# Performance work log

Measured on AMD Instinct MI355X. Metric: run time of the kernel, lower is better.

## Reference

```python
import jax, jax.numpy as jnp
import numpy as np

# ---- static problem constants ----
LX, LY, D, P = 6, 6, 4, 2          # PEPS grid, bond dim, phys dim
CHI = 16                            # max_bond for boundary truncation
ETA = 0.1                           # nn_eta
NS = LX * LY                        # n_sites = 36
E, HEADS, HID = 128, 8, 512         # embed_dim, attn_heads, nn_hidden_dim
B = 2048                            # batch

def _shapes():
    s = []
    for i in range(LX):
        for j in range(LY):
            s.append((1 if i == 0 else D, 1 if i == LX - 1 else D,
                      1 if j == 0 else D, 1 if j == LY - 1 else D, P))
    return s

SHAPES = _shapes()                              # per-site (u,d,l,r,p)
SIZES = [int(np.prod(s)) for s in SHAPES]       # param_sizes in PointwiseBackflow
OFFS = np.concatenate([[0], np.cumsum(SIZES)])
TOTAL = int(OFFS[-1])
MAXS = max(SIZES)                               # 512


def setup_inputs() -> dict:
    key = jax.random.key(0)
    ks = jax.random.split(key, 12)
    f = jnp.float32
    return {
        "x": jax.random.randint(ks[0], (B, NS), 0, P),
        "ftn_flat": jax.random.normal(ks[1], (TOTAL,), f) * 0.25,
        "emb": jax.random.normal(ks[2], (P, E), f) * 0.1,
        "pos": jax.random.normal(ks[3], (NS, E), f) * 0.1,
        "Wqkv": jax.random.normal(ks[4], (E, 3 * E), f) / np.sqrt(E),
        "bqkv": jnp.zeros((3 * E,), f),
        "Wo": jax.random.normal(ks[5], (E, E), f) / np.sqrt(E),
        "bo": jnp.zeros((E,), f),
        "W1": jax.random.normal(ks[6], (E, HID), f) / np.sqrt(E),
        "b1": jnp.zeros((HID,), f),
        "W2": jax.random.normal(ks[7], (HID, MAXS), f) * 0.02,
        "b2": jnp.zeros((MAXS,), f),
    }


def _compress(mps, chi):
    """Canonicalize (top->bottom) then SVD-truncate (bottom->top) an open MPS.
    mps[i] has shape (bond_up, bond_down, phys); cutoff=0, max_bond=chi."""
    mps = list(mps)
    n = len(mps)
    for i in range(n - 1):
        a, b, p = mps[i].shape
        U, S, Vh = jnp.linalg.svd(mps[i].transpose(0, 2, 1).reshape(a * p, b),
                                  full_matrices=False)
        k = U.shape[1]
        mps[i] = U.reshape(a, p, k).transpose(0, 2, 1)
        mps[i + 1] = jnp.einsum('kb,bcp->kcp', S[:, None] * Vh, mps[i + 1])
    for i in range(n - 1, 0, -1):
        a, b, p = mps[i].shape
        U, S, Vh = jnp.linalg.svd(mps[i].reshape(a, b * p), full_matrices=False)
        k = min(chi, int(S.shape[0]))
        mps[i] = Vh[:k].reshape(k, b, p)
        mps[i - 1] = jnp.einsum('xap,ak->xkp', mps[i - 1], U[:, :k] * S[:k])
    return mps


def _absorb(bt, t, side):
    # bt: (a, c, q) boundary-MPS tensor, t: (u, d, l, r) site tensor
    if side == 'r':   # contract q with site's l, new phys = r
        out = jnp.einsum('acl,udlr->aucdr', bt, t)
    else:             # contract q with site's r, new phys = l
        out = jnp.einsum('acr,udlr->aucdl', bt, t)
    a, u, c, d, p = out.shape
    return out.reshape(a * u, c * d, p)


def _contract_one(xi, vec):
    """Amplitude of one config: select phys indices, then boundary contraction
    from ymin over cols [0, LY//2-1] and from ymax over cols [LY//2, LY-1]."""
    grid = []
    for i in range(LX):
        row = []
        for j in range(LY):
            k_ = i * LY + j
            t = vec[OFFS[k_]:OFFS[k_ + 1]].reshape(SHAPES[k_])
            row.append(jnp.take(t, xi[k_], axis=-1))  # (u,d,l,r)
        grid.append(row)
    # left boundary MPS (phys = right bond)
    lmps = [grid[i][0][:, :, 0, :] for i in range(LX)]
    for j in range(1, LY // 2):
        lmps = _compress([_absorb(lmps[i], grid[i][j], 'r') for i in range(LX)], CHI)
    # right boundary MPS (phys = left bond)
    rmps = [grid[i][LY - 1][:, :, :, 0] for i in range(LX)]
    for j in range(LY - 2, LY // 2 - 1, -1):
        rmps = _compress([_absorb(rmps[i], grid[i][j], 'l') for i in range(LX)], CHI)
    # zip the two boundary MPS
    M = jnp.ones((1, 1), vec.dtype)
    for i in range(LX):
        M = jnp.einsum('xy,xap,ybp->ab', M, lmps[i], rmps[i])
    return M[0, 0]


def _forward(x, ftn_flat, emb, pos, Wqkv, bqkv, Wo, bo, W1, b1, W2, b2):
    bsz = x.shape[0]
    h = emb[x] + pos                                   # [B, NS, E]
    qkv = h @ Wqkv + bqkv
    q, k, v = jnp.split(qkv, 3, axis=-1)
    dh = E // HEADS
    q = q.reshape(bsz, NS, HEADS, dh)
    k = k.reshape(bsz, NS, HEADS, dh)
    v = v.reshape(bsz, NS, HEADS, dh)
    att = jax.nn.softmax(jnp.einsum('bqhd,bkhd->bhqk', q, k) / np.sqrt(dh), axis=-1)
    o = jnp.einsum('bhqk,bkhd->bqhd', att, v).reshape(bsz, NS, E)
    h = h + o @ Wo + bo                                # attn block output
    raw = jax.nn.gelu(h @ W1 + b1, approximate=False) @ W2 + b2  # [B, NS, MAXS]
    # PointwiseBackflow: per-site trim + concat
    nn_out = jnp.concatenate([raw[:, i, :SIZES[i]] for i in range(NS)], axis=1)
    vecs = ftn_flat[None, :] + ETA * nn_out            # [B, TOTAL]
    return jax.vmap(_contract_one)(x, vecs)            # [B]


def reference(x, ftn_flat, emb, pos, Wqkv, bqkv, Wo, bo, W1, b1, W2, b2):
    return _forward(x, ftn_flat, emb, pos, Wqkv, bqkv, Wo, bo, W1, b1, W2, b2)
```

## Files before the change

### kernel.cpp

```cpp
#include <hip/hip_runtime.h>
#include <math.h>


#define BSZ   2048
#define NS    36
#define EMB   128
#define NHEAD 8
#define DH    16
#define HIDD  512
#define TOTV  10368

typedef float f16v __attribute__((ext_vector_type(16)));

__device__ __forceinline__ float hsum16(f16v v) {
    float a = (v[0] + v[1]) + (v[2] + v[3]);
    float b = (v[4] + v[5]) + (v[6] + v[7]);
    float c = (v[8] + v[9]) + (v[10] + v[11]);
    float d = (v[12] + v[13]) + (v[14] + v[15]);
    return (a + b) + (c + d);
}

__constant__ int c_offs[37] = {
    0,32,160,288,416,544,576,
    704,1216,1728,2240,2752,2880,
    3008,3520,4032,4544,5056,5184,
    5312,5824,6336,6848,7360,7488,
    7616,8128,8640,9152,9664,9792,
    9824,9952,10080,10208,10336,10368};

__constant__ int c_ps[84] = {
    0,1,2,3,4,5,
    6,7,7,7,7,8,8,8,8,9,9,9,9,10,10,10,10,11,
    12,13,13,13,13,14,14,14,14,15,15,15,15,16,16,16,16,17,
    18,19,19,19,19,20,20,20,20,21,21,21,21,22,22,22,22,23,
    24,25,25,25,25,26,26,26,26,27,27,27,27,28,28,28,28,29,
    30,31,32,33,34,35};
__constant__ int c_pc[84] = {
    0,0,0,0,0,0,
    0,0,1,2,3,0,1,2,3,0,1,2,3,0,1,2,3,0,
    0,0,1,2,3,0,1,2,3,0,1,2,3,0,1,2,3,0,
    0,0,1,2,3,0,1,2,3,0,1,2,3,0,1,2,3,0,
    0,0,1,2,3,0,1,2,3,0,1,2,3,0,1,2,3,0,
    0,0,0,0,0,0};

__global__ __launch_bounds__(256) void k_embed(const int* __restrict__ x,
        const float* __restrict__ emb, const float* __restrict__ pos,
        float* __restrict__ h) {
    int idx = blockIdx.x * 256 + threadIdx.x;
    if (idx >= BSZ * NS * EMB) return;
    int e = idx & (EMB - 1);
    int g = idx >> 7;
    int s = g % NS;
    h[idx] = emb[x[g] * EMB + e] + pos[s * EMB + e];
}

__global__ __launch_bounds__(256) void k_qkv(const float* __restrict__ h,
        const float* __restrict__ Wqkv, const float* __restrict__ bqkv,
        float* __restrict__ qkv) {
    __shared__ float As[64 * 132];
    __shared__ float Ws[32 * 132];
    int tid = threadIdx.x;
    int chunk = blockIdx.x;
    int tok0 = blockIdx.y * 64;
    int tx = tid & 15, ty = tid >> 4;
    for (int idx = tid; idx < 64 * 128; idx += 256) {
        int t = idx >> 7, k = idx & 127;
        As[t * 132 + k] = h[(size_t)(tok0 + t) * EMB + k];
    }
    float acc[4][8];
    #pragma unroll
    for (int i = 0; i < 4; ++i)
        #pragma unroll
        for (int q = 0; q < 8; ++q) acc[i][q] = 0.f;
    for (int ks = 0; ks < 4; ++ks) {
        __syncthreads();
        for (int idx = tid; idx < 32 * 128; idx += 256) {
            int kk = idx >> 7, c = idx & 127;
            Ws[kk * 132 + c] = Wqkv[(size_t)(ks * 32 + kk) * 384 + chunk * 128 + c];
        }
        __syncthreads();
        #pragma unroll 4
        for (int kk = 0; kk < 32; ++kk) {
            float4 w0 = *(const float4*)&Ws[kk * 132 + tx * 8];
            float4 w1 = *(const float4*)&Ws[kk * 132 + tx * 8 + 4];
            #pragma unroll
            for (int i = 0; i < 4; ++i) {
                float a = As[(ty * 4 + i) * 132 + ks * 32 + kk];
                acc[i][0] += a * w0.x; acc[i][1] += a * w0.y;
                acc[i][2] += a * w0.z; acc[i][3] += a * w0.w;
                acc[i][4] += a * w1.x; acc[i][5] += a * w1.y;
                acc[i][6] += a * w1.z; acc[i][7] += a * w1.w;
            }
        }
    }
    #pragma unroll
    for (int i = 0; i < 4; ++i) {
        size_t base = (size_t)(tok0 + ty * 4 + i) * 384 + chunk * 128 + tx * 8;
        #pragma unroll
        for (int q = 0; q < 8; ++q)
            qkv[base + q] = acc[i][q] + bqkv[chunk * 128 + tx * 8 + q];
    }
}

__global__ __launch_bounds__(256) void k_attnc(float* __restrict__ qkv) {
    __shared__ float qs[4][NS * 17];
    __shared__ float ks_[4][NS * 17];
    __shared__ float vs[4][NS * 17];
    __shared__ float S[4][NS * 37];
    int wid = threadIdx.x >> 6, lane = threadIdx.x & 63;
    int m = blockIdx.x * 4 + wid;
    int b = m >> 3, hd = m & 7;
    float* Q = qkv + (size_t)b * NS * 384 + hd * DH;
    for (int idx = lane; idx < NS * DH; idx += 64) {
        int t = idx >> 4, d = idx & 15;
        qs[wid][t * 17 + d]  = Q[t * 384 + d];
        ks_[wid][t * 17 + d] = Q[t * 384 + 128 + d];
        vs[wid][t * 17 + d]  = Q[t * 384 + 256 + d];
    }
    __syncthreads();
    for (int idx = lane; idx < NS * NS; idx += 64) {
        int qp = idx / NS, kp = idx - qp * NS;
        float acc = 0.f;
        #pragma unroll
        for (int d = 0; d < DH; ++d)
            acc += qs[wid][qp * 17 + d] * ks_[wid][kp * 17 + d];
        S[wid][qp * 37 + kp] = acc * 0.25f;
    }
    __syncthreads();
    if (lane < NS) {
        float mx = -1e30f;
        for (int j = 0; j < NS; ++j) mx = fmaxf(mx, S[wid][lane * 37 + j]);
        float z = 0.f;
        for (int j = 0; j < NS; ++j) {
            float e = expf(S[wid][lane * 37 + j] - mx);
            S[wid][lane * 37 + j] = e; z += e;
        }
        float inv = 1.f / z;
        for (int j = 0; j < NS; ++j) S[wid][lane * 37 + j] *= inv;
    }
    __syncthreads();
    for (int idx = lane; idx < NS * DH; idx += 64) {
        int qp = idx >> 4, d = idx & 15;
        float acc = 0.f;
        for (int kp = 0; kp < NS; ++kp)
            acc += S[wid][qp * 37 + kp] * vs[wid][kp * 17 + d];
        Q[qp * 384 + d] = acc;
    }
}

__global__ __launch_bounds__(256) void k_oproj(const float* __restrict__ qkv,
        const float* __restrict__ Wo, const float* __restrict__ bo,
        float* __restrict__ h) {
    __shared__ float As[64 * 132];
    __shared__ float Ws[32 * 132];
    int tid = threadIdx.x;
    int tok0 = blockIdx.x * 64;
    int tx = tid & 15, ty = tid >> 4;
    for (int idx = tid; idx < 64 * 128; idx += 256) {
        int t = idx >> 7, k = idx & 127;
        As[t * 132 + k] = qkv[(size_t)(tok0 + t) * 384 + k];
    }
    float acc[4][8];
    #pragma unroll
    for (int i = 0; i < 4; ++i)
        #pragma unroll
        for (int q = 0; q < 8; ++q) acc[i][q] = 0.f;
    for (int ks = 0; ks < 4; ++ks) {
        __syncthreads();
        for (int idx = tid; idx < 32 * 128; idx += 256) {
            int kk = idx >> 7, c = idx & 127;
            Ws[kk * 132 + c] = Wo[(size_t)(ks * 32 + kk) * EMB + c];
        }
        __syncthreads();
        #pragma unroll 4
        for (int kk = 0; kk < 32; ++kk) {
            float4 w0 = *(const float4*)&Ws[kk * 132 + tx * 8];
            float4 w1 = *(const float4*)&Ws[kk * 132 + tx * 8 + 4];
            #pragma unroll
            for (int i = 0; i < 4; ++i) {
                float a = As[(ty * 4 + i) * 132 + ks * 32 + kk];
                acc[i][0] += a * w0.x; acc[i][1] += a * w0.y;
                acc[i][2] += a * w0.z; acc[i][3] += a * w0.w;
                acc[i][4] += a * w1.x; acc[i][5] += a * w1.y;
                acc[i][6] += a * w1.z; acc[i][7] += a * w1.w;
            }
        }
    }
    #pragma unroll
    for (int i = 0; i < 4; ++i) {
        size_t base = (size_t)(tok0 + ty * 4 + i) * EMB + tx * 8;
        #pragma unroll
        for (int q = 0; q < 8; ++q)
            h[base + q] = h[base + q] + acc[i][q] + bo[tx * 8 + q];
    }
}

__global__ __launch_bounds__(256) void k_gemm1(const float* __restrict__ h,
        const float* __restrict__ W1, const float* __restrict__ b1,
        float* __restrict__ Hm) {
    __shared__ float As[64 * 132];
    __shared__ float Ws[32 * 132];
    int tid = threadIdx.x;
    int chunk = blockIdx.x;
    int tok0 = blockIdx.y * 64;
    int tx = tid & 15, ty = tid >> 4;
    for (int idx = tid; idx < 64 * 128; idx += 256) {
        int t = idx >> 7, k = idx & 127;
        As[t * 132 + k] = h[(size_t)(tok0 + t) * EMB + k];
    }
    float acc[4][8];
    #pragma unroll
    for (int i = 0; i < 4; ++i)
        #pragma unroll
        for (int q = 0; q < 8; ++q) acc[i][q] = 0.f;
    for (int ks = 0; ks < 4; ++ks) {
        __syncthreads();
        for (int idx = tid; idx < 32 * 128; idx += 256) {
            int kk = idx >> 7, c = idx & 127;
            Ws[kk * 132 + c] = W1[(size_t)(ks * 32 + kk) * HIDD + chunk * 128 + c];
        }
        __syncthreads();
        #pragma unroll 4
        for (int kk = 0; kk < 32; ++kk) {
            float4 w0 = *(const float4*)&Ws[kk * 132 + tx * 8];
            float4 w1 = *(const float4*)&Ws[kk * 132 + tx * 8 + 4];
            #pragma unroll
            for (int i = 0; i < 4; ++i) {
                float a = As[(ty * 4 + i) * 132 + ks * 32 + kk];
                acc[i][0] += a * w0.x; acc[i][1] += a * w0.y;
                acc[i][2] += a * w0.z; acc[i][3] += a * w0.w;
                acc[i][4] += a * w1.x; acc[i][5] += a * w1.y;
                acc[i][6] += a * w1.z; acc[i][7] += a * w1.w;
            }
        }
    }
    #pragma unroll
    for (int i = 0; i < 4; ++i) {
        size_t base = (size_t)(tok0 + ty * 4 + i) * HIDD + chunk * 128 + tx * 8;
        #pragma unroll
        for (int q = 0; q < 8; ++q) {
            float a = acc[i][q] + b1[chunk * 128 + tx * 8 + q];
            Hm[base + q] = 0.5f * a * (1.f + erff(a * 0.70710678118654752f));
        }
    }
}

__global__ __launch_bounds__(256) void k_gemm2(const float* __restrict__ Hm,
        const float* __restrict__ W2, const float* __restrict__ b2,
        const float* __restrict__ ftn, float* __restrict__ vecs, int e8) {
    __shared__ float As[64 * 33];
    __shared__ float Ws[32 * 132];
    int tid = threadIdx.x;
    int pair = blockIdx.x;
    int s = c_ps[pair], chunk = c_pc[pair];
    int b0 = blockIdx.y * 64;
    int off = c_offs[s], size = c_offs[s + 1] - off;
    int tx = tid & 15, ty = tid >> 4;
    float acc[4][8];
    #pragma unroll
    for (int i = 0; i < 4; ++i)
        #pragma unroll
        for (int q = 0; q < 8; ++q) acc[i][q] = 0.f;
    for (int ks = 0; ks < 16; ++ks) {
        __syncthreads();
        for (int idx = tid; idx < 64 * 32; idx += 256) {
            int t = idx >> 5, kk = idx & 31;
            As[t * 33 + kk] = Hm[(size_t)((b0 + t) * NS + s) * HIDD + ks * 32 + kk];
        }
        for (int idx = tid; idx < 32 * 128; idx += 256) {
            int kk = idx >> 7, c = idx & 127;
            Ws[kk * 132 + c] = W2[(size_t)(ks * 32 + kk) * HIDD + chunk * 128 + c];
        }
        __syncthreads();
        #pragma unroll 4
        for (int kk = 0; kk < 32; ++kk) {
            float4 w0 = *(const float4*)&Ws[kk * 132 + tx * 8];
            float4 w1 = *(const float4*)&Ws[kk * 132 + tx * 8 + 4];
            #pragma unroll
            for (int i = 0; i < 4; ++i) {
                float a = As[(ty * 4 + i) * 33 + kk];
                acc[i][0] += a * w0.x; acc[i][1] += a * w0.y;
                acc[i][2] += a * w0.z; acc[i][3] += a * w0.w;
                acc[i][4] += a * w1.x; acc[i][5] += a * w1.y;
                acc[i][6] += a * w1.z; acc[i][7] += a * w1.w;
            }
        }
    }
    #pragma unroll
    for (int i = 0; i < 4; ++i) {
        int bg = e8 * 256 + b0 + ty * 4 + i;
        #pragma unroll
        for (int q = 0; q < 8; ++q) {
            int col = chunk * 128 + tx * 8 + q;
            if (col < size) {
                float o = acc[i][q] + b2[col];
                vecs[(size_t)bg * TOTV + off + col] = ftn[off + col] + 0.1f * o;
            }
        }
    }
}

__device__ __forceinline__ float* build_half(const float* __restrict__ vb,
        const int* __restrict__ xb, int side, int upper,
        float* cur, float* fre, float* ts0, float* ts1, float* ts2, int tid) {
    if (tid == 0) cur[0] = 1.0f;
    __syncthreads();
    int bd = 1, lgbd = 0;
    for (int t = 0; t < 3; ++t) {
        int xd = t ? 4 : 1, lgxd = t ? 2 : 0;
        int j = side ? (5 - t) : t;
        int rows[3];
        rows[0] = upper ? 0 : 5; rows[1] = upper ? 1 : 4; rows[2] = upper ? 2 : 3;
        for (int role = 0; role < 3; ++role) {
            int i = rows[role];
            int dd = (i < 5) ? 4 : 1, dl = (j > 0) ? 4 : 1, dr = (j < 5) ? 4 : 1;
            int su = dd * dl * dr * 2, sd = dl * dr * 2, sl = dr * 2, sr = 2;
            int xstr = side ? sr : sl, ystr = side ? sl : sr;
            int base = c_offs[i * 6 + j] + xb[i * 6 + j];
            if (role == 0) {
                int astr = upper ? sd : su;
                int n = 4 * xd * 4;
                for (int idx = tid; idx < n; idx += 256) {
                    int y = idx & 3, xx = (idx >> 2) & (xd - 1), a = idx >> (2 + lgxd);
                    ts0[idx] = vb[base + a * astr + xx * xstr + y * ystr];
                }
            } else if (role == 1) {
                int astr = upper ? su : sd, cstr = upper ? sd : su;
                int n = 16 * xd * 4;
                for (int idx = tid; idx < n; idx += 256) {
                    int y = idx & 3, xx = (idx >> 2) & (xd - 1);
                    int c = (idx >> (2 + lgxd)) & 3, a = idx >> (4 + lgxd);
                    ts1[idx] = vb[base + a * astr + c * cstr + xx * xstr + y * ystr];
                }
            } else {
                int cstr = upper ? su : sd, bstr = upper ? sd : su;
                int n = 16 * xd * 4;
                for (int idx = tid; idx < n; idx += 256) {
                    int y = idx & 3, xx = (idx >> 2) & (xd - 1);
                    int bb = (idx >> (2 + lgxd)) & 3, c = idx >> (4 + lgxd);
                    ts2[idx] = vb[base + c * cstr + bb * bstr + xx * xstr + y * ystr];
                }
            }
        }
        __syncthreads();
        int n1 = 16 * xd * xd * bd;
        for (int idx = tid; idx < n1; idx += 256) {
            int bt = idx & (bd - 1);
            int r = idx >> lgbd;
            int x2 = r & (xd - 1); r >>= lgxd;
            int x1 = r & (xd - 1); r >>= lgxd;
            int a = r & 3, y0 = r >> 2;
            float s2 = 0.f;
            for (int x0 = 0; x0 < xd; ++x0)
                s2 += cur[(((((x0 << lgxd) | x1) << lgxd) | x2) << lgbd) | bt]
                    * ts0[(((a << lgxd) | x0) << 2) | y0];
            fre[idx] = s2;
        }
        __syncthreads();
        int n2 = 64 * xd * bd;
        for (int idx = tid; idx < n2; idx += 256) {
            int bt = idx & (bd - 1);
            int r = idx >> lgbd;
            int x2 = r & (xd - 1); r >>= lgxd;
            int c = r & 3, y1 = (r >> 2) & 3, y0 = r >> 4;
            float s2 = 0.f;
            for (int a = 0; a < 4; ++a)
                for (int x1 = 0; x1 < xd; ++x1)
                    s2 += fre[((((((((y0 << 2) | a) << lgxd) | x1) << lgxd) | x2)) << lgbd) | bt]
                        * ts1[((((a * 4 + c) << lgxd) | x1) << 2) | y1];
            cur[idx] = s2;
        }
        __syncthreads();
        int n3 = 256 * bd;
        for (int idx = tid; idx < n3; idx += 256) {
            int bn = idx & (4 * bd - 1);
            int bt = bn >> 2, bb = bn & 3;
            int r = idx >> (lgbd + 2);
            int y2 = r & 3, y1 = (r >> 2) & 3, y0 = r >> 4;
            float s2 = 0.f;
            for (int c = 0; c < 4; ++c)
                for (int x2 = 0; x2 < xd; ++x2)
                    s2 += cur[((((((y0 << 2) | y1) << 2 | c) << lgxd) | x2) << lgbd) | bt]
                        * ts2[((((c * 4 + bb) << lgxd) | x2) << 2) | y2];
            fre[idx] = s2;
        }
        __syncthreads();
        float* tmp = cur; cur = fre; fre = tmp;
        bd <<= 2; lgbd += 2;
    }
    return cur;
}

__global__ __launch_bounds__(256) void k_build(const float* __restrict__ vecs,
        const int* __restrict__ x, float* __restrict__ psi) {
    __shared__ float X1[4096], X2[4096], X3[4096];
    __shared__ float ts0[64], ts1[256], ts2[256];
    int m = blockIdx.x;
    int b = m >> 1, side = m & 1;
    int tid = threadIdx.x;
    const float* vb = vecs + (size_t)b * TOTV;
    const int* xb = x + b * NS;
    float* A  = build_half(vb, xb, side, 1, X1, X2, ts0, ts1, ts2, tid);
    float* Bt = build_half(vb, xb, side, 0, X1, X3, ts0, ts1, ts2, tid);
    float* po = psi + (size_t)m * 4096;
    for (int idx = tid; idx < 4096; idx += 256) {
        int u = idx >> 6, l = idx & 63;
        const float4* a4 = (const float4*)(A + u * 64);
        const float4* b4 = (const float4*)(Bt + l * 64);
        float s2 = 0.f;
        #pragma unroll
        for (int q = 0; q < 16; ++q) {
            float4 av = a4[q], bv = b4[q];
            s2 += av.x * bv.x + av.y * bv.y + av.z * bv.z + av.w * bv.w;
        }
        po[idx] = s2;
    }
}

__global__ __launch_bounds__(64, 1) void k_svd(const float* __restrict__ psi,
                                               float* __restrict__ wv) {
    __shared__ __align__(16) float qlds[2][64 * 20];
    int lane = threadIdx.x;
    int mA = blockIdx.x * 2;
    const float* PA = psi + (size_t)mA * 4096;
    const float* PB = PA + 4096;
    f16v a0, a1, a2, a3, b0, b1, b2, b3;
    #pragma unroll
    for (int r = 0; r < 16; ++r) a0[r] = PA[r * 64 + lane];
    #pragma unroll
    for (int r = 0; r < 16; ++r) a1[r] = PA[(r + 16) * 64 + lane];
    #pragma unroll
    for (int r = 0; r < 16; ++r) a2[r] = PA[(r + 32) * 64 + lane];
    #pragma unroll
    for (int r = 0; r < 16; ++r) a3[r] = PA[(r + 48) * 64 + lane];
    #pragma unroll
    for (int r = 0; r < 16; ++r) b0[r] = PB[r * 64 + lane];
    #pragma unroll
    for (int r = 0; r < 16; ++r) b1[r] = PB[(r + 16) * 64 + lane];
    #pragma unroll
    for (int r = 0; r < 16; ++r) b2[r] = PB[(r + 32) * 64 + lane];
    #pragma unroll
    for (int r = 0; r < 16; ++r) b3[r] = PB[(r + 48) * 64 + lane];

    bool actA = true, actB = true;
    for (int sweep = 0; sweep < 5; ++sweep) {
        if (!actA && !actB) break;
        float nA = 0.f, nB = 0.f;
        if (actA) {
            f16v nv = a0 * a0 + a1 * a1 + a2 * a2 + a3 * a3;
            nA = hsum16(nv);
        }
        if (actB) {
            f16v nv = b0 * b0 + b1 * b1 + b2 * b2 + b3 * b3;
            nB = hsum16(nv);
        }
        bool bigA = false, bigB = false;
        for (int mm = 1; mm < 64; ++mm) {
            int partner = lane ^ mm;
            if (actA) {
                f16v p0, p1, p2, p3;
                #pragma unroll
                for (int r = 0; r < 16; ++r) p0[r] = __shfl(a0[r], partner);
                #pragma unroll
                for (int r = 0; r < 16; ++r) p1[r] = __shfl(a1[r], partner);
                #pragma unroll
                for (int r = 0; r < 16; ++r) p2[r] = __shfl(a2[r], partner);
                #pragma unroll
                for (int r = 0; r < 16; ++r) p3[r] = __shfl(a3[r], partner);
                f16v gv = a0 * p0 + a1 * p1 + a2 * p2 + a3 * p3;
                float gam = hsum16(gv);
                float beta2 = __shfl(nA, partner);
                float scale = sqrtf(fmaxf(nA * beta2, 0.f));
                bool rot = fabsf(gam) > 1e-5f * scale;
                bool big = fabsf(gam) > 4e-3f * scale;
                if (__ballot(big) != 0ull) bigA = true;
                if (__ballot(rot) != 0ull) {
                    float c = 1.f, s = 0.f;
                    if (rot) {
                        float zeta = (nA - beta2) / (2.f * gam);
                        float sgn = (zeta > 0.f) ? 1.f :
                                    ((zeta < 0.f) ? -1.f : ((lane < partner) ? 1.f : -1.f));
                        float tt = sgn / (fabsf(zeta) + sqrtf(1.f + zeta * zeta));
                        c = 1.f / sqrtf(1.f + tt * tt);
                        s = c * tt;
                    }
                    a0 = c * a0 + s * p0;
                    a1 = c * a1 + s * p1;
                    a2 = c * a2 + s * p2;
                    a3 = c * a3 + s * p3;
                    nA = c * c * nA + s * s * beta2 + 2.f * c * s * gam;
                }
            }
            if (actB) {
                f16v p0, p1, p2, p3;
                #pragma unroll
                for (int r = 0; r < 16; ++r) p0[r] = __shfl(b0[r], partner);
                #pragma unroll
                for (int r = 0; r < 16; ++r) p1[r] = __shfl(b1[r], partner);
                #pragma unroll
                for (int r = 0; r < 16; ++r) p2[r] = __shfl(b2[r], partner);
                #pragma unroll
                for (int r = 0; r < 16; ++r) p3[r] = __shfl(b3[r], partner);
                f16v gv = b0 * p0 + b1 * p1 + b2 * p2 + b3 * p3;
                float gam = hsum16(gv);
                float beta2 = __shfl(nB, partner);
                float scale = sqrtf(fmaxf(nB * beta2, 0.f));
                bool rot = fabsf(gam) > 1e-5f * scale;
                bool big = fabsf(gam) > 4e-3f * scale;
                if (__ballot(big) != 0ull) bigB = true;
                if (__ballot(rot) != 0ull) {
                    float c = 1.f, s = 0.f;
                    if (rot) {
                        float zeta = (nB - beta2) / (2.f * gam);
                        float sgn = (zeta > 0.f) ? 1.f :
                                    ((zeta < 0.f) ? -1.f : ((lane < partner) ? 1.f : -1.f));
                        float tt = sgn / (fabsf(zeta) + sqrtf(1.f + zeta * zeta));
                        c = 1.f / sqrtf(1.f + tt * tt);
                        s = c * tt;
                    }
                    b0 = c * b0 + s * p0;
                    b1 = c * b1 + s * p1;
                    b2 = c * b2 + s * p2;
                    b3 = c * b3 + s * p3;
                    nB = c * c * nB + s * s * beta2 + 2.f * c * s * gam;
                }
            }
        }
        actA = actA && bigA;
        actB = actB && bigB;
    }

    {
        f16v ne = a0 * a0 + a1 * a1 + a2 * a2 + a3 * a3;
        float n2e = hsum16(ne);
        int rank = 0;
        for (int j = 0; j < 64; ++j) {
            float nj = __shfl(n2e, j);
            if (nj > n2e || (nj == n2e && j < lane)) ++rank;
        }
        float inv = (n2e > 1e-30f) ? 1.f / sqrtf(n2e) : 0.f;
        if (rank < 16) {
            #pragma unroll
            for (int r = 0; r < 16; ++r) {
                qlds[0][r * 20 + rank]        = a0[r] * inv;
                qlds[0][(r + 16) * 20 + rank] = a1[r] * inv;
                qlds[0][(r + 32) * 20 + rank] = a2[r] * inv;
                qlds[0][(r + 48) * 20 + rank] = a3[r] * inv;
            }
        }
    }
    {
        f16v ne = b0 * b0 + b1 * b1 + b2 * b2 + b3 * b3;
        float n2e = hsum16(ne);
        int rank = 0;
        for (int j = 0; j < 64; ++j) {
            float nj = __shfl(n2e, j);
            if (nj > n2e || (nj == n2e && j < lane)) ++rank;
        }
        float inv = (n2e > 1e-30f) ? 1.f / sqrtf(n2e) : 0.f;
        if (rank < 16) {
            #pragma unroll
            for (int r = 0; r < 16; ++r) {
                qlds[1][r * 20 + rank]        = b0[r] * inv;
                qlds[1][(r + 16) * 20 + rank] = b1[r] * inv;
                qlds[1][(r + 32) * 20 + rank] = b2[r] * inv;
                qlds[1][(r + 48) * 20 + rank] = b3[r] * inv;
            }
        }
    }
    __syncthreads();
    #pragma unroll
    for (int g = 0; g < 2; ++g) {
        const float* P = g ? PB : PA;
        float* o = wv + (size_t)(mA + g) * 2048;
        #pragma unroll
        for (int k = 0; k < 16; ++k) o[k * 64 + lane] = qlds[g][lane * 20 + k];
        f16v t;
        #pragma unroll
        for (int k = 0; k < 16; ++k) t[k] = 0.f;
        for (int r = 0; r < 64; ++r) {
            float pr = P[r * 64 + lane];
            const float4* q4 = (const float4*)&qlds[g][r * 20];
            float4 a = q4[0], b = q4[1], cc = q4[2], d = q4[3];
            t[0]  += a.x  * pr; t[1]  += a.y  * pr; t[2]  += a.z  * pr; t[3]  += a.w  * pr;
            t[4]  += b.x  * pr; t[5]  += b.y  * pr; t[6]  += b.z  * pr; t[7]  += b.w  * pr;
            t[8]  += cc.x * pr; t[9]  += cc.y * pr; t[10] += cc.z * pr; t[11] += cc.w * pr;
            t[12] += d.x  * pr; t[13] += d.y  * pr; t[14] += d.z  * pr; t[15] += d.w  * pr;
        }
        #pragma unroll
        for (int k = 0; k < 16; ++k) o[1024 + k * 64 + lane] = t[k];
    }
}

__global__ __launch_bounds__(256) void k_amp(const float* __restrict__ wv,
                                             float* __restrict__ out) {
    __shared__ float s[4096];
    __shared__ float part[4];
    int b = blockIdx.x, tid = threadIdx.x;
    const float* src = wv + (size_t)b * 4096;
    for (int i = tid; i < 4096; i += 256) s[i] = src[i];
    __syncthreads();
    int k = tid >> 4, mm = tid & 15;
    const float* WL = s;
    const float* VL = s + 1024;
    const float* WR = s + 2048;
    const float* VR = s + 3072;
    float du = 0.f, dv = 0.f;
    for (int r = 0; r < 64; ++r) {
        du += WL[k * 64 + r] * WR[mm * 64 + r];
        dv += VL[k * 64 + r] * VR[mm * 64 + r];
    }
    float p = du * dv;
    for (int off = 32; off > 0; off >>= 1) p += __shfl_down(p, off);
    if ((tid & 63) == 0) part[tid >> 6] = p;
    __syncthreads();
    if (tid == 0) out[b] = part[0] + part[1] + part[2] + part[3];
}

extern "C" void kernel_launch(void* const* d_in, const int* in_sizes, int n_in,
                              void* d_out, int out_size, void* d_ws, size_t ws_size,
                              hipStream_t stream) {
    const int*   x    = (const int*)d_in[0];
    const float* ftn  = (const float*)d_in[1];
    const float* emb  = (const float*)d_in[2];
    const float* pos  = (const float*)d_in[3];
    const float* Wqkv = (const float*)d_in[4];
    const float* bqkv = (const float*)d_in[5];
    const float* Wo   = (const float*)d_in[6];
    const float* bo   = (const float*)d_in[7];
    const float* W1   = (const float*)d_in[8];
    const float* b1   = (const float*)d_in[9];
    const float* W2   = (const float*)d_in[10];
    const float* b2   = (const float*)d_in[11];
    float* out = (float*)d_out;
    float* ws  = (float*)d_ws;

    float* h    = ws;
    float* Hm_e = ws + 9437184;
    float* psi  = ws;
    float* vecs = ws + 16777216;
    float* qkv  = ws + 16777216;
    float* wv   = ws + 16777216 + 21233664;

    hipLaunchKernelGGL(k_embed, dim3((BSZ * NS * EMB + 255) / 256), dim3(256), 0, stream,
                       x, emb, pos, h);
    hipLaunchKernelGGL(k_qkv, dim3(3, 1152), dim3(256), 0, stream,
                       h, Wqkv, bqkv, qkv);
    hipLaunchKernelGGL(k_attnc, dim3(BSZ * NHEAD / 4), dim3(256), 0, stream, qkv);
    hipLaunchKernelGGL(k_oproj, dim3(1152), dim3(256), 0, stream,
                       qkv, Wo, bo, h);
    for (int e8 = 0; e8 < 8; ++e8) {
        const float* h_e = h + (size_t)e8 * 9216 * EMB;
        hipLaunchKernelGGL(k_gemm1, dim3(4, 144), dim3(256), 0, stream,
                           h_e, W1, b1, Hm_e);
        hipLaunchKernelGGL(k_gemm2, dim3(84, 4), dim3(256), 0, stream,
                           Hm_e, W2, b2, ftn, vecs, e8);
    }
    hipLaunchKernelGGL(k_build, dim3(2 * BSZ), dim3(256), 0, stream, vecs, x, psi);
    hipLaunchKernelGGL(k_svd, dim3(BSZ), dim3(64), 0, stream, psi, wv);
    hipLaunchKernelGGL(k_amp, dim3(BSZ), dim3(256), 0, stream, wv, out);
}
```

Measured before the change: 2.929 ms.

## Build upper and lower boundary halves concurrently with split thread groups

The k_build kernel now splits its 256 threads into two groups of 128, each building one half (upper or lower) of the boundary environment at the same time in separate shared buffers, instead of building the two halves one after the other with all threads. This halves the number of sequential barrier-separated stages and avoids serial dependence between halves. It raises shared memory use per block (four 16KB buffers instead of three), which may reduce occupancy. Both groups still hit the same block-wide __syncthreads, and each group uses the same number of stages, so the barriers line up. The final result is read from the second buffer of each half, which relies on three swaps ending in that buffer.

```diff
diff --git a/kernel.cpp b/kernel.cpp
--- a/kernel.cpp
+++ b/kernel.cpp
@@ -300,10 +300,10 @@
     }
 }
 
-__device__ __forceinline__ float* build_half(const float* __restrict__ vb,
+__device__ __forceinline__ void build_half128(const float* __restrict__ vb,
         const int* __restrict__ xb, int side, int upper,
-        float* cur, float* fre, float* ts0, float* ts1, float* ts2, int tid) {
-    if (tid == 0) cur[0] = 1.0f;
+        float* cur, float* fre, float* ts0, float* ts1, float* ts2, int t128) {
+    if (t128 == 0) cur[0] = 1.0f;
     __syncthreads();
     int bd = 1, lgbd = 0;
     for (int t = 0; t < 3; ++t) {
@@ -320,14 +320,14 @@
             if (role == 0) {
                 int astr = upper ? sd : su;
                 int n = 4 * xd * 4;
-                for (int idx = tid; idx < n; idx += 256) {
+                for (int idx = t128; idx < n; idx += 128) {
                     int y = idx & 3, xx = (idx >> 2) & (xd - 1), a = idx >> (2 + lgxd);
                     ts0[idx] = vb[base + a * astr + xx * xstr + y * ystr];
                 }
             } else if (role == 1) {
                 int astr = upper ? su : sd, cstr = upper ? sd : su;
                 int n = 16 * xd * 4;
-                for (int idx = tid; idx < n; idx += 256) {
+                for (int idx = t128; idx < n; idx += 128) {
                     int y = idx & 3, xx = (idx >> 2) & (xd - 1);
                     int c = (idx >> (2 + lgxd)) & 3, a = idx >> (4 + lgxd);
                     ts1[idx] = vb[base + a * astr + c * cstr + xx * xstr + y * ystr];
@@ -335,7 +335,7 @@
             } else {
                 int cstr = upper ? su : sd, bstr = upper ? sd : su;
                 int n = 16 * xd * 4;
-                for (int idx = tid; idx < n; idx += 256) {
+                for (int idx = t128; idx < n; idx += 128) {
                     int y = idx & 3, xx = (idx >> 2) & (xd - 1);
                     int bb = (idx >> (2 + lgxd)) & 3, c = idx >> (4 + lgxd);
                     ts2[idx] = vb[base + c * cstr + bb * bstr + xx * xstr + y * ystr];
@@ -344,7 +344,7 @@
         }
         __syncthreads();
         int n1 = 16 * xd * xd * bd;
-        for (int idx = tid; idx < n1; idx += 256) {
+        for (int idx = t128; idx < n1; idx += 128) {
             int bt = idx & (bd - 1);
             int r = idx >> lgbd;
             int x2 = r & (xd - 1); r >>= lgxd;
@@ -358,7 +358,7 @@
         }
         __syncthreads();
         int n2 = 64 * xd * bd;
-        for (int idx = tid; idx < n2; idx += 256) {
+        for (int idx = t128; idx < n2; idx += 128) {
             int bt = idx & (bd - 1);
             int r = idx >> lgbd;
             int x2 = r & (xd - 1); r >>= lgxd;
@@ -372,7 +372,7 @@
         }
         __syncthreads();
         int n3 = 256 * bd;
-        for (int idx = tid; idx < n3; idx += 256) {
+        for (int idx = t128; idx < n3; idx += 128) {
             int bn = idx & (4 * bd - 1);
             int bt = bn >> 2, bb = bn & 3;
             int r = idx >> (lgbd + 2);
@@ -388,20 +388,25 @@
         float* tmp = cur; cur = fre; fre = tmp;
         bd <<= 2; lgbd += 2;
     }
-    return cur;
 }
 
 __global__ __launch_bounds__(256) void k_build(const float* __restrict__ vecs,
         const int* __restrict__ x, float* __restrict__ psi) {
-    __shared__ float X1[4096], X2[4096], X3[4096];
-    __shared__ float ts0[64], ts1[256], ts2[256];
+    __shared__ float XU1[4096], XU2[4096], XL1[4096], XL2[4096];
+    __shared__ float tsU0[64], tsU1[256], tsU2[256];
+    __shared__ float tsL0[64], tsL1[256], tsL2[256];
     int m = blockIdx.x;
     int b = m >> 1, side = m & 1;
     int tid = threadIdx.x;
+    int half = tid >> 7, t128 = tid & 127;
     const float* vb = vecs + (size_t)b * TOTV;
     const int* xb = x + b * NS;
-    float* A  = build_half(vb, xb, side, 1, X1, X2, ts0, ts1, ts2, tid);
-    float* Bt = build_half(vb, xb, side, 0, X1, X3, ts0, ts1, ts2, tid);
+    build_half128(vb, xb, side, half ? 0 : 1,
+                  half ? XL1 : XU1, half ? XL2 : XU2,
+                  half ? tsL0 : tsU0, half ? tsL1 : tsU1, half ? tsL2 : tsU2,
+                  t128);
+    const float* A  = XU2;
+    const float* Bt = XL2;
     float* po = psi + (size_t)m * 4096;
     for (int idx = tid; idx < 4096; idx += 256) {
         int u = idx >> 6, l = idx & 63;
```

After: 2.995 ms. +2.3%, slower.
